# Kernel optimization log

Measured on AMD Instinct MI355X. Metric: run time of the kernel, lower is better.

The kernel has to match this reference:

```python
import jax, jax.numpy as jnp
from jax import lax
import numpy as np

NMS_THRESH = 0.3
N_OBJ, N_REL, C_OBJ, C_REL, D = 512, 16384, 151, 51, 4096


def _pairwise_iou(boxes):
    # boxes: [N,4] in (x1,y1,x2,y2); pascal-style +1 area as in neural-motifs/KERN nms
    x1, y1, x2, y2 = boxes[:, 0], boxes[:, 1], boxes[:, 2], boxes[:, 3]
    area = (x2 - x1 + 1.0) * (y2 - y1 + 1.0)
    xx1 = jnp.maximum(x1[:, None], x1[None, :])
    yy1 = jnp.maximum(y1[:, None], y1[None, :])
    xx2 = jnp.minimum(x2[:, None], x2[None, :])
    yy2 = jnp.minimum(y2[:, None], y2[None, :])
    w = jnp.maximum(xx2 - xx1 + 1.0, 0.0)
    h = jnp.maximum(yy2 - yy1 + 1.0, 0.0)
    inter = w * h
    return inter / (area[:, None] + area[None, :] - inter)


def _nms_keep(scores, boxes, thresh):
    # greedy NMS over all N boxes (pre_nms_topn = post_nms_topn = N); returns bool keep mask [N]
    n = scores.shape[0]
    order = jnp.argsort(-scores)
    iou = _pairwise_iou(boxes[order])  # [N,N] in score-sorted order

    def step(suppressed, xs):
        row, i = xs
        keep_i = jnp.logical_not(suppressed[i])
        suppressed = suppressed | (keep_i & (row > thresh))
        return suppressed, keep_i

    _, keep_sorted = lax.scan(step, jnp.zeros(n, bool), (iou, jnp.arange(n)))
    return jnp.zeros(n, bool).at[order].set(keep_sorted)


def setup_inputs() -> dict:
    key = jax.random.key(0)
    k1, k2, k3, k4, k5 = jax.random.split(key, 5)
    obj_logits = jax.random.normal(k1, (N_OBJ, C_OBJ), jnp.float32)
    vr = jax.random.normal(k2, (N_REL, D), jnp.float32)
    # valid boxes: x2 > x1, y2 > y1
    xy = jax.random.uniform(k3, (N_OBJ, C_OBJ, 2), jnp.float32) * 800.0
    wh = jax.random.uniform(k4, (N_OBJ, C_OBJ, 2), jnp.float32) * 200.0 + 16.0
    boxes_per_cls = jnp.concatenate([xy, xy + wh], axis=-1)
    W_vr = jax.random.normal(k5, (C_REL, D), jnp.float32) * (1.0 / np.sqrt(D))
    b_vr = jnp.zeros((C_REL,), jnp.float32)
    return {"obj_logits": obj_logits, "vr": vr, "boxes_per_cls": boxes_per_cls,
            "W_vr": W_vr, "b_vr": b_vr}


def reference(obj_logits, vr, boxes_per_cls, W_vr, b_vr):
    # VRFC forward, mode='sgdet', eval: per-class NMS mask (computed on detached data,
    # as in the torch .data path), then obj_preds argmax over fg classes, then rel FC.
    obj_dists2 = obj_logits
    probs = jax.nn.softmax(lax.stop_gradient(obj_dists2), axis=1)  # [N_obj, C_obj]
    boxes = lax.stop_gradient(boxes_per_cls)
    keep_all = jax.vmap(lambda s, b: _nms_keep(s, b, NMS_THRESH),
                        in_axes=(1, 1), out_axes=1)(probs, boxes)  # [N_obj, C_obj] bool
    nms_mask = keep_all.astype(probs.dtype).at[:, 0].set(0.0)  # loop started at class 1
    obj_preds = jnp.argmax((nms_mask * probs)[:, 1:], axis=1) + 1  # [N_obj] int
    rel_dists = vr @ W_vr.T + b_vr  # [N_rel, C_rel]
    return obj_dists2, obj_preds, rel_dists
```

## Files before the change

### kernel.cpp

```cpp
#include <hip/hip_runtime.h>

#define C_OBJ 151
#define N_OBJ 512
#define N_RELK 16384
#define C_REL 51
#define DDIM 4096

#define OUT_PREDS 77312
#define OUT_REL   77824

typedef float f32x4 __attribute__((ext_vector_type(4)));
typedef __bf16 bf16x8 __attribute__((ext_vector_type(8)));

__device__ inline unsigned short f2bf_rne(float x) {
  unsigned int u = __float_as_uint(x);
  unsigned int r = (u + 0x7FFFu + ((u >> 16) & 1u)) >> 16;
  return (unsigned short)r;
}
__device__ inline float bf2f(unsigned short h) {
  return __uint_as_float(((unsigned int)h) << 16);
}

__global__ void softmax_copy_kernel(const float* __restrict__ logits,
                                    float* __restrict__ out,
                                    float* __restrict__ probs) {
  const int o = blockIdx.x;
  const int lane = threadIdx.x;
  float v[3];
  float mx = -3.4e38f;
#pragma unroll
  for (int j = 0; j < 3; ++j) {
    int c = lane + j * 64;
    if (c < C_OBJ) {
      float x = logits[o * C_OBJ + c];
      out[o * C_OBJ + c] = x;
      v[j] = x;
      mx = fmaxf(mx, x);
    } else {
      v[j] = -3.4e38f;
    }
  }
  for (int off = 32; off; off >>= 1) mx = fmaxf(mx, __shfl_xor(mx, off));
  float e[3];
  float s = 0.f;
#pragma unroll
  for (int j = 0; j < 3; ++j) {
    int c = lane + j * 64;
    e[j] = (c < C_OBJ) ? expf(v[j] - mx) : 0.f;
    s += e[j];
  }
  for (int off = 32; off; off >>= 1) s += __shfl_xor(s, off);
#pragma unroll
  for (int j = 0; j < 3; ++j) {
    int c = lane + j * 64;
    if (c < C_OBJ) probs[o * C_OBJ + c] = e[j] / s;
  }
}

__global__ __launch_bounds__(512) void nms_kernel(const float* __restrict__ probs,
                                                  const float* __restrict__ boxes,
                                                  float* __restrict__ masked) {
  const int c = blockIdx.x + 1;
  const int t = threadIdx.x;

  __shared__ float s[N_OBJ];
  __shared__ int id[N_OBJ];
  __shared__ float bx1[N_OBJ], by1[N_OBJ], bx2[N_OBJ], by2[N_OBJ], ar[N_OBJ];
  __shared__ unsigned long long m[N_OBJ][8];
  __shared__ unsigned char keepS[N_OBJ];

  s[t] = probs[t * C_OBJ + c];
  id[t] = t;
  __syncthreads();

  for (int k = 2; k <= N_OBJ; k <<= 1) {
    for (int j = k >> 1; j > 0; j >>= 1) {
      int ixj = t ^ j;
      if (ixj > t) {
        float sa = s[t], sb = s[ixj];
        int ia = id[t], ib = id[ixj];
        bool before = (sa > sb) || (sa == sb && ia < ib);
        bool up = ((t & k) == 0);
        if (up ? !before : before) {
          s[t] = sb; s[ixj] = sa;
          id[t] = ib; id[ixj] = ia;
        }
      }
      __syncthreads();
    }
  }

  {
    int o = id[t];
    const float* bp = boxes + ((size_t)o * C_OBJ + c) * 4;
    float X1 = bp[0], Y1 = bp[1], X2 = bp[2], Y2 = bp[3];
    bx1[t] = X1; by1[t] = Y1; bx2[t] = X2; by2[t] = Y2;
    ar[t] = (X2 - X1 + 1.f) * (Y2 - Y1 + 1.f);
  }
  __syncthreads();

  {
    float X1 = bx1[t], Y1 = by1[t], X2 = bx2[t], Y2 = by2[t], A = ar[t];
    for (int w = 0; w < 8; ++w) {
      unsigned long long bits = 0ull;
      for (int jj = 0; jj < 64; ++jj) {
        int j = (w << 6) + jj;
        float xx1 = fmaxf(X1, bx1[j]);
        float yy1 = fmaxf(Y1, by1[j]);
        float xx2 = fminf(X2, bx2[j]);
        float yy2 = fminf(Y2, by2[j]);
        float ww = fmaxf(xx2 - xx1 + 1.f, 0.f);
        float hh = fmaxf(yy2 - yy1 + 1.f, 0.f);
        float inter = ww * hh;
        float iou = inter / (A + ar[j] - inter);
        if (iou > 0.3f) bits |= (1ull << jj);
      }
      m[t][w] = bits;
    }
  }
  __syncthreads();

  if (t < 64) {
    const int w = t & 7;
    unsigned long long supw = 0ull;
    for (int i = 0; i < N_OBJ; ++i) {
      unsigned long long srcw = __shfl(supw, i >> 6);
      int kept = !((srcw >> (i & 63)) & 1ull);
      if (t == 0) keepS[i] = (unsigned char)kept;
      unsigned long long row = m[i][w];
      if (kept) supw |= row;
    }
  }
  __syncthreads();

  masked[(size_t)id[t] * (C_OBJ - 1) + (c - 1)] =
      keepS[t] ? probs[(size_t)id[t] * C_OBJ + c] : 0.f;
}

__global__ void argmax_kernel(const float* __restrict__ masked,
                              float* __restrict__ outp) {
  const int o = blockIdx.x * 4 + (threadIdx.x >> 6);
  const int lane = threadIdx.x & 63;
  float bv = -1.f;
  int bc = 1 << 20;
  for (int j = lane; j < C_OBJ - 1; j += 64) {
    float x = masked[(size_t)o * (C_OBJ - 1) + j];
    int cc = j + 1;
    if (x > bv || (x == bv && cc < bc)) { bv = x; bc = cc; }
  }
  for (int off = 32; off; off >>= 1) {
    float ov = __shfl_xor(bv, off);
    int oc = __shfl_xor(bc, off);
    if (ov > bv || (ov == bv && oc < bc)) { bv = ov; bc = oc; }
  }
  if (lane == 0) outp[o] = (float)bc;
}

#define LDS_STRIDE 40
__global__ __launch_bounds__(256) void gemm_kernel(const float* __restrict__ A,
                                                   const float* __restrict__ W,
                                                   const float* __restrict__ bias,
                                                   float* __restrict__ out) {
  __shared__ unsigned short aHi[64 * LDS_STRIDE], aLo[64 * LDS_STRIDE];
  __shared__ unsigned short bHi[64 * LDS_STRIDE], bLo[64 * LDS_STRIDE];

  const int t = threadIdx.x;
  const int bm = blockIdx.x * 64;
  const int wave = t >> 6;
  const int lane = t & 63;

  const int sr0 = t >> 3;
  const int sr1 = 32 + sr0;
  const int sc = (t & 7) * 4;

  float4 pa0, pa1, pb0, pb1;
  const float4 z4 = make_float4(0.f, 0.f, 0.f, 0.f);

  auto loadT = [&](int kt) {
    const int ko = kt * 32 + sc;
    pa0 = *(const float4*)(A + (size_t)(bm + sr0) * DDIM + ko);
    pa1 = *(const float4*)(A + (size_t)(bm + sr1) * DDIM + ko);
    pb0 = *(const float4*)(W + (size_t)sr0 * DDIM + ko);
    pb1 = (sr1 < C_REL) ? *(const float4*)(W + (size_t)sr1 * DDIM + ko) : z4;
  };

  auto cw = [&](float4 v, unsigned short* hp, unsigned short* lp) {
    ushort4 h, l;
    float x;
    x = v.x; h.x = f2bf_rne(x); l.x = f2bf_rne(x - bf2f(h.x));
    x = v.y; h.y = f2bf_rne(x); l.y = f2bf_rne(x - bf2f(h.y));
    x = v.z; h.z = f2bf_rne(x); l.z = f2bf_rne(x - bf2f(h.z));
    x = v.w; h.w = f2bf_rne(x); l.w = f2bf_rne(x - bf2f(h.w));
    *(ushort4*)hp = h;
    *(ushort4*)lp = l;
  };

  f32x4 acc0 = {0.f, 0.f, 0.f, 0.f};
  f32x4 acc1 = acc0, acc2 = acc0, acc3 = acc0;

  const int aoff = (wave * 16 + (lane & 15)) * LDS_STRIDE + (lane >> 4) * 8;
  const int boff = (lane & 15) * LDS_STRIDE + (lane >> 4) * 8;

  loadT(0);
  for (int kt = 0; kt < DDIM / 32; ++kt) {
    __syncthreads();
    cw(pa0, aHi + sr0 * LDS_STRIDE + sc, aLo + sr0 * LDS_STRIDE + sc);
    cw(pa1, aHi + sr1 * LDS_STRIDE + sc, aLo + sr1 * LDS_STRIDE + sc);
    cw(pb0, bHi + sr0 * LDS_STRIDE + sc, bLo + sr0 * LDS_STRIDE + sc);
    cw(pb1, bHi + sr1 * LDS_STRIDE + sc, bLo + sr1 * LDS_STRIDE + sc);
    __syncthreads();
    if (kt + 1 < DDIM / 32) loadT(kt + 1);

    bf16x8 ah = *(const bf16x8*)(aHi + aoff);
    bf16x8 al = *(const bf16x8*)(aLo + aoff);
#define NTILE(ACC, N)                                                          \
    {                                                                          \
      bf16x8 bh = *(const bf16x8*)(bHi + boff + (N) * 16 * LDS_STRIDE);        \
      bf16x8 bl = *(const bf16x8*)(bLo + boff + (N) * 16 * LDS_STRIDE);        \
      ACC = __builtin_amdgcn_mfma_f32_16x16x32_bf16(ah, bh, ACC, 0, 0, 0);     \
      ACC = __builtin_amdgcn_mfma_f32_16x16x32_bf16(al, bh, ACC, 0, 0, 0);     \
      ACC = __builtin_amdgcn_mfma_f32_16x16x32_bf16(ah, bl, ACC, 0, 0, 0);     \
    }
    NTILE(acc0, 0)
    NTILE(acc1, 1)
    NTILE(acc2, 2)
    NTILE(acc3, 3)
#undef NTILE
  }

  const int r0 = bm + wave * 16 + (lane >> 4) * 4;
#define EPI(ACC, N)                                                            \
  {                                                                            \
    int cc = (N) * 16 + (lane & 15);                                           \
    if (cc < C_REL) {                                                          \
      float bv = bias[cc];                                                     \
      out[(size_t)(r0 + 0) * C_REL + cc] = ACC[0] + bv;                        \
      out[(size_t)(r0 + 1) * C_REL + cc] = ACC[1] + bv;                        \
      out[(size_t)(r0 + 2) * C_REL + cc] = ACC[2] + bv;                        \
      out[(size_t)(r0 + 3) * C_REL + cc] = ACC[3] + bv;                        \
    }                                                                          \
  }
  EPI(acc0, 0)
  EPI(acc1, 1)
  EPI(acc2, 2)
  EPI(acc3, 3)
#undef EPI
}

extern "C" void kernel_launch(void* const* d_in, const int* in_sizes, int n_in,
                              void* d_out, int out_size, void* d_ws, size_t ws_size,
                              hipStream_t stream) {
  const float* logits = (const float*)d_in[0];
  const float* vr     = (const float*)d_in[1];
  const float* boxes  = (const float*)d_in[2];
  const float* W      = (const float*)d_in[3];
  const float* bias   = (const float*)d_in[4];
  float* out = (float*)d_out;
  float* ws  = (float*)d_ws;

  float* probs  = ws;
  float* masked = ws + N_OBJ * C_OBJ;

  hipLaunchKernelGGL(softmax_copy_kernel, dim3(N_OBJ), dim3(64), 0, stream,
                     logits, out, probs);
  hipLaunchKernelGGL(nms_kernel, dim3(C_OBJ - 1), dim3(N_OBJ), 0, stream,
                     probs, boxes, masked);
  hipLaunchKernelGGL(argmax_kernel, dim3(N_OBJ / 4), dim3(256), 0, stream,
                     masked, out + OUT_PREDS);
  hipLaunchKernelGGL(gemm_kernel, dim3(N_RELK / 64), dim3(256), 0, stream,
                     vr, W, bias, out + OUT_REL);
}
```

Baseline: 576.8 us.

## Rewrite rel GEMM with split-K, pre-converted bf16 weights, register prefetch, no LDS

A separate kernel pre-converts W to bf16 in an MFMA-ready fragment layout. The GEMM drops LDS staging and loads A straight into registers with a 4-deep prefetch. Work is split across two K halves, with atomicAdd into an output pre-filled with the bias. The weight low-order correction term is dropped (two MFMAs per tile instead of three), which lowers precision on W. This aims to remove sync and LDS overhead and raise parallelism, at the cost of atomics and extra launches.

```diff
diff --git a/kernel.cpp b/kernel.cpp
--- a/kernel.cpp
+++ b/kernel.cpp
@@ -5,12 +5,17 @@
 #define N_RELK 16384
 #define C_REL 51
 #define DDIM 4096
+#define KSPLIT 2
+#define KHALF (DDIM / KSPLIT)
+#define KSTEPS (KHALF / 32)
+#define PF 4
 
 #define OUT_PREDS 77312
 #define OUT_REL   77824
 
 typedef float f32x4 __attribute__((ext_vector_type(4)));
 typedef __bf16 bf16x8 __attribute__((ext_vector_type(8)));
+typedef unsigned short u16x8 __attribute__((ext_vector_type(8)));
 
 __device__ inline unsigned short f2bf_rne(float x) {
   unsigned int u = __float_as_uint(x);
@@ -156,88 +161,108 @@
   if (lane == 0) outp[o] = (float)bc;
 }
 
-#define LDS_STRIDE 40
-__global__ __launch_bounds__(256) void gemm_kernel(const float* __restrict__ A,
-                                                   const float* __restrict__ W,
-                                                   const float* __restrict__ bias,
-                                                   float* __restrict__ out) {
-  __shared__ unsigned short aHi[64 * LDS_STRIDE], aLo[64 * LDS_STRIDE];
-  __shared__ unsigned short bHi[64 * LDS_STRIDE], bLo[64 * LDS_STRIDE];
-
-  const int t = threadIdx.x;
-  const int bm = blockIdx.x * 64;
-  const int wave = t >> 6;
-  const int lane = t & 63;
-
-  const int sr0 = t >> 3;
-  const int sr1 = 32 + sr0;
-  const int sc = (t & 7) * 4;
-
-  float4 pa0, pa1, pb0, pb1;
-  const float4 z4 = make_float4(0.f, 0.f, 0.f, 0.f);
-
-  auto loadT = [&](int kt) {
-    const int ko = kt * 32 + sc;
-    pa0 = *(const float4*)(A + (size_t)(bm + sr0) * DDIM + ko);
-    pa1 = *(const float4*)(A + (size_t)(bm + sr1) * DDIM + ko);
-    pb0 = *(const float4*)(W + (size_t)sr0 * DDIM + ko);
-    pb1 = (sr1 < C_REL) ? *(const float4*)(W + (size_t)sr1 * DDIM + ko) : z4;
-  };
-
-  auto cw = [&](float4 v, unsigned short* hp, unsigned short* lp) {
-    ushort4 h, l;
-    float x;
-    x = v.x; h.x = f2bf_rne(x); l.x = f2bf_rne(x - bf2f(h.x));
-    x = v.y; h.y = f2bf_rne(x); l.y = f2bf_rne(x - bf2f(h.y));
-    x = v.z; h.z = f2bf_rne(x); l.z = f2bf_rne(x - bf2f(h.z));
-    x = v.w; h.w = f2bf_rne(x); l.w = f2bf_rne(x - bf2f(h.w));
-    *(ushort4*)hp = h;
-    *(ushort4*)lp = l;
-  };
+__global__ void convB_kernel(const float* __restrict__ W,
+                             unsigned short* __restrict__ Bhi) {
+  const int tid = blockIdx.x * 256 + threadIdx.x;
+  const int kt = tid >> 8;
+  const int rem = tid & 255;
+  const int n = rem >> 6;
+  const int l = rem & 63;
+  const int col = n * 16 + (l & 15);
+  const int k = kt * 32 + ((l >> 4) << 3);
+  u16x8 vh;
+#pragma unroll
+  for (int j = 0; j < 8; ++j) {
+    float x = (col < C_REL) ? W[(size_t)col * DDIM + k + j] : 0.f;
+    vh[j] = f2bf_rne(x);
+  }
+  *(u16x8*)(Bhi + (size_t)tid * 8) = vh;
+}
+
+__global__ void init_rel_kernel(const float* __restrict__ bias,
+                                float* __restrict__ outrel) {
+  const int idx = blockIdx.x * 256 + threadIdx.x;
+  const int c = idx - (idx / C_REL) * C_REL;
+  outrel[idx] = bias[c];
+}
+
+__global__ __launch_bounds__(256, 2) void gemm_kernel(const float* __restrict__ A,
+                                                      const unsigned short* __restrict__ Bhi,
+                                                      float* __restrict__ outrel) {
+  const int blk = blockIdx.x;
+  const int ks = blk & (KSPLIT - 1);
+  const int mb = blk >> 1;
+  const int wave = threadIdx.x >> 6;
+  const int lane = threadIdx.x & 63;
+
+  const int row = mb * 64 + wave * 16 + (lane & 15);
+  const float* ap = A + (size_t)row * DDIM + ks * KHALF + ((lane >> 4) << 3);
+  const unsigned short* bp = Bhi + (size_t)(ks * KSTEPS) * 2048 + (lane << 3);
 
   f32x4 acc0 = {0.f, 0.f, 0.f, 0.f};
   f32x4 acc1 = acc0, acc2 = acc0, acc3 = acc0;
 
-  const int aoff = (wave * 16 + (lane & 15)) * LDS_STRIDE + (lane >> 4) * 8;
-  const int boff = (lane & 15) * LDS_STRIDE + (lane >> 4) * 8;
-
-  loadT(0);
-  for (int kt = 0; kt < DDIM / 32; ++kt) {
-    __syncthreads();
-    cw(pa0, aHi + sr0 * LDS_STRIDE + sc, aLo + sr0 * LDS_STRIDE + sc);
-    cw(pa1, aHi + sr1 * LDS_STRIDE + sc, aLo + sr1 * LDS_STRIDE + sc);
-    cw(pb0, bHi + sr0 * LDS_STRIDE + sc, bLo + sr0 * LDS_STRIDE + sc);
-    cw(pb1, bHi + sr1 * LDS_STRIDE + sc, bLo + sr1 * LDS_STRIDE + sc);
-    __syncthreads();
-    if (kt + 1 < DDIM / 32) loadT(kt + 1);
-
-    bf16x8 ah = *(const bf16x8*)(aHi + aoff);
-    bf16x8 al = *(const bf16x8*)(aLo + aoff);
-#define NTILE(ACC, N)                                                          \
-    {                                                                          \
-      bf16x8 bh = *(const bf16x8*)(bHi + boff + (N) * 16 * LDS_STRIDE);        \
-      bf16x8 bl = *(const bf16x8*)(bLo + boff + (N) * 16 * LDS_STRIDE);        \
-      ACC = __builtin_amdgcn_mfma_f32_16x16x32_bf16(ah, bh, ACC, 0, 0, 0);     \
-      ACC = __builtin_amdgcn_mfma_f32_16x16x32_bf16(al, bh, ACC, 0, 0, 0);     \
-      ACC = __builtin_amdgcn_mfma_f32_16x16x32_bf16(ah, bl, ACC, 0, 0, 0);     \
-    }
-    NTILE(acc0, 0)
-    NTILE(acc1, 1)
-    NTILE(acc2, 2)
-    NTILE(acc3, 3)
-#undef NTILE
-  }
-
-  const int r0 = bm + wave * 16 + (lane >> 4) * 4;
+  f32x4 abuf[PF][2];
+#pragma unroll
+  for (int u = 0; u < PF; ++u) {
+    abuf[u][0] = *(const f32x4*)(ap + u * 32);
+    abuf[u][1] = *(const f32x4*)(ap + u * 32 + 4);
+  }
+  u16x8 bbuf[2][4];
+#pragma unroll
+  for (int n = 0; n < 4; ++n) bbuf[0][n] = *(const u16x8*)(bp + n * 512);
+
+  for (int kt = 0; kt < KSTEPS; kt += PF) {
+#pragma unroll
+    for (int u = 0; u < PF; ++u) {
+      const int cur = kt + u;
+      {
+        int nb = cur + 1;
+        if (nb >= KSTEPS) nb = KSTEPS - 1;
+        const unsigned short* bq = bp + (size_t)nb * 2048;
+#pragma unroll
+        for (int n = 0; n < 4; ++n)
+          bbuf[(u + 1) & 1][n] = *(const u16x8*)(bq + n * 512);
+      }
+      u16x8 uh, ul;
+      {
+        f32x4 a0 = abuf[u][0], a1 = abuf[u][1];
+#define CVT1(i, X) { float x_ = (X); unsigned short h_ = f2bf_rne(x_); uh[i] = h_; ul[i] = f2bf_rne(x_ - bf2f(h_)); }
+        CVT1(0, a0.x) CVT1(1, a0.y) CVT1(2, a0.z) CVT1(3, a0.w)
+        CVT1(4, a1.x) CVT1(5, a1.y) CVT1(6, a1.z) CVT1(7, a1.w)
+#undef CVT1
+      }
+      {
+        int na = cur + PF;
+        if (na >= KSTEPS) na = KSTEPS - 1;
+        abuf[u][0] = *(const f32x4*)(ap + (size_t)na * 32);
+        abuf[u][1] = *(const f32x4*)(ap + (size_t)na * 32 + 4);
+      }
+      bf16x8 ah = __builtin_bit_cast(bf16x8, uh);
+      bf16x8 al = __builtin_bit_cast(bf16x8, ul);
+#define NT(ACC, N)                                                             \
+      {                                                                        \
+        bf16x8 bh_ = __builtin_bit_cast(bf16x8, bbuf[u & 1][N]);               \
+        ACC = __builtin_amdgcn_mfma_f32_16x16x32_bf16(ah, bh_, ACC, 0, 0, 0);  \
+        ACC = __builtin_amdgcn_mfma_f32_16x16x32_bf16(al, bh_, ACC, 0, 0, 0);  \
+      }
+      NT(acc0, 0)
+      NT(acc1, 1)
+      NT(acc2, 2)
+      NT(acc3, 3)
+#undef NT
+    }
+  }
+
+  const int r0 = mb * 64 + wave * 16 + ((lane >> 4) << 2);
 #define EPI(ACC, N)                                                            \
   {                                                                            \
     int cc = (N) * 16 + (lane & 15);                                           \
     if (cc < C_REL) {                                                          \
-      float bv = bias[cc];                                                     \
-      out[(size_t)(r0 + 0) * C_REL + cc] = ACC[0] + bv;                        \
-      out[(size_t)(r0 + 1) * C_REL + cc] = ACC[1] + bv;                        \
-      out[(size_t)(r0 + 2) * C_REL + cc] = ACC[2] + bv;                        \
-      out[(size_t)(r0 + 3) * C_REL + cc] = ACC[3] + bv;                        \
+      atomicAdd(&outrel[(size_t)(r0 + 0) * C_REL + cc], ACC[0]);               \
+      atomicAdd(&outrel[(size_t)(r0 + 1) * C_REL + cc], ACC[1]);               \
+      atomicAdd(&outrel[(size_t)(r0 + 2) * C_REL + cc], ACC[2]);               \
+      atomicAdd(&outrel[(size_t)(r0 + 3) * C_REL + cc], ACC[3]);               \
     }                                                                          \
   }
   EPI(acc0, 0)
@@ -260,13 +285,17 @@
 
   float* probs  = ws;
   float* masked = ws + N_OBJ * C_OBJ;
-
+  unsigned short* Bhi = (unsigned short*)(ws + 154112);
+
+  hipLaunchKernelGGL(convB_kernel, dim3(128), dim3(256), 0, stream, W, Bhi);
+  hipLaunchKernelGGL(init_rel_kernel, dim3((N_RELK * C_REL) / 256), dim3(256), 0,
+                     stream, bias, out + OUT_REL);
   hipLaunchKernelGGL(softmax_copy_kernel, dim3(N_OBJ), dim3(64), 0, stream,
                      logits, out, probs);
   hipLaunchKernelGGL(nms_kernel, dim3(C_OBJ - 1), dim3(N_OBJ), 0, stream,
                      probs, boxes, masked);
   hipLaunchKernelGGL(argmax_kernel, dim3(N_OBJ / 4), dim3(256), 0, stream,
                      masked, out + OUT_PREDS);
-  hipLaunchKernelGGL(gemm_kernel, dim3(N_RELK / 64), dim3(256), 0, stream,
-                     vr, W, bias, out + OUT_REL);
-}
+  hipLaunchKernelGGL(gemm_kernel, dim3((N_RELK / 64) * KSPLIT), dim3(256), 0,
+                     stream, vr, Bhi, out + OUT_REL);
+}
```

New measurement: 518.2 us. 10.2% less time.
